# Kernel optimization log

Hardware: AMD Instinct MI355X
Metric: run time of the kernel (lower is better)

Reference implementation:

```python
import jax, jax.numpy as jnp
import numpy as np
import math

D_MODEL = 512
NHEAD = 8
HEAD_DIM = D_MODEL // NHEAD
MAX_REL = 128
B, T, S = 4, 2048, 2048


def setup_inputs() -> dict:
    key = jax.random.key(0)
    ks = jax.random.split(key, 16)
    sc = 1.0 / math.sqrt(D_MODEL)
    inp = {
        "query": jax.random.normal(ks[0], (B, T, D_MODEL), jnp.float32),
        "key": jax.random.normal(ks[1], (B, S, D_MODEL), jnp.float32),
        "value": jax.random.normal(ks[2], (B, S, D_MODEL), jnp.float32),
        "Wq": jax.random.normal(ks[3], (D_MODEL, D_MODEL), jnp.float32) * sc,
        "bq": jnp.zeros((D_MODEL,), jnp.float32),
        "Wk": jax.random.normal(ks[4], (D_MODEL, D_MODEL), jnp.float32) * sc,
        "bk": jnp.zeros((D_MODEL,), jnp.float32),
        "Wv": jax.random.normal(ks[5], (D_MODEL, D_MODEL), jnp.float32) * sc,
        "bv": jnp.zeros((D_MODEL,), jnp.float32),
        "Wo": jax.random.normal(ks[6], (D_MODEL, D_MODEL), jnp.float32) * sc,
        "bo": jnp.zeros((D_MODEL,), jnp.float32),
        "rel_emb": jax.random.normal(ks[7], (2 * MAX_REL + 1, NHEAD), jnp.float32) * 0.02,
    }
    return inp


def reference(query, key, value, Wq, bq, Wk, bk, Wv, bv, Wo, bo, rel_emb):
    # linear projections (torch Linear: x @ W.T + b), split heads -> [B,H,T,Dh]
    def proj(x, W, b, L):
        return (x @ W.T + b).reshape(B, L, NHEAD, HEAD_DIM).transpose(0, 2, 1, 3)

    q = proj(query, Wq, bq, T)
    k = proj(key, Wk, bk, S)
    v = proj(value, Wv, bv, S)

    scores = jnp.einsum("bhtd,bhsd->bhts", q, k) / math.sqrt(HEAD_DIM)

    # relative position bias lookup: rel[t,s] = clamp(t-s) + max_rel -> [H,T,S]
    rel = jnp.arange(T)[:, None] - jnp.arange(S)[None, :]
    rel = jnp.clip(rel, -MAX_REL, MAX_REL) + MAX_REL
    bias = rel_emb[rel].transpose(2, 0, 1)  # [H,T,S]
    scores = scores + bias[None]

    w = jax.nn.softmax(scores, axis=-1)  # dropout p used in eval mode -> identity
    out = jnp.einsum("bhts,bhsd->bhtd", w, v)
    out = out.transpose(0, 2, 1, 3).reshape(B, T, D_MODEL)
    return out @ Wo.T + bo
```

## Files before the change

kernel.cpp:

```cpp
#include <hip/hip_runtime.h>

typedef __attribute__((ext_vector_type(4))) float f32x4;
typedef __attribute__((ext_vector_type(16))) float f32x16;
typedef __attribute__((ext_vector_type(4))) unsigned short u16x4;
typedef __attribute__((ext_vector_type(8))) unsigned short u16x8;
typedef __attribute__((ext_vector_type(4))) unsigned int u32x4;
typedef __attribute__((ext_vector_type(8))) __bf16 bf16x8;

#define SZX_E ((size_t)4 * 2048 * 512)
#define SZW_E ((size_t)512 * 512)

__device__ __forceinline__ unsigned short f2bf(float f) {
  unsigned int u = __builtin_bit_cast(unsigned int, f);
  u += 0x7fffu + ((u >> 16) & 1u);
  return (unsigned short)(u >> 16);
}

__device__ __forceinline__ bf16x8 ld_bf8(const unsigned short* p) {
  return __builtin_bit_cast(bf16x8, *(const u16x8*)p);
}

__device__ __forceinline__ f32x4 mfma16(bf16x8 a, bf16x8 b, f32x4 c) {
  return __builtin_amdgcn_mfma_f32_16x16x32_bf16(a, b, c, 0, 0, 0);
}

__device__ __forceinline__ f32x16 mfma32(bf16x8 a, bf16x8 b, f32x16 c) {
  return __builtin_amdgcn_mfma_f32_32x32x16_bf16(a, b, c, 0, 0, 0);
}

__device__ __forceinline__ unsigned int cvt_pk_bf16(float lo, float hi) {
  unsigned int r;
  asm("v_cvt_pk_bf16_f32 %0, %1, %2" : "=v"(r) : "v"(lo), "v"(hi));
  return r;
}

__device__ __forceinline__ void plane32_swap(unsigned int& a, unsigned int& b) {
  asm("v_permlane32_swap_b32 %0, %1" : "+v"(a), "+v"(b));
}

__device__ __forceinline__ float exp2_fast(float x) {
  float r;
  asm("v_exp_f32 %0, %1" : "=v"(r) : "v"(x));
  return r;
}

__device__ __forceinline__ void gload16(const void* g, void* l) {
  __builtin_amdgcn_global_load_lds(
      (const __attribute__((address_space(1))) unsigned int*)g,
      (__attribute__((address_space(3))) unsigned int*)l, 16, 0, 0);
}

#define VBAR4 do { \
    asm volatile("s_waitcnt vmcnt(4)" ::: "memory"); \
    __builtin_amdgcn_sched_barrier(0); \
    __builtin_amdgcn_s_barrier(); \
    __builtin_amdgcn_sched_barrier(0); \
  } while (0)
#define VBAR0 do { \
    asm volatile("s_waitcnt vmcnt(0)" ::: "memory"); \
    __builtin_amdgcn_sched_barrier(0); \
    __builtin_amdgcn_s_barrier(); \
    __builtin_amdgcn_sched_barrier(0); \
  } while (0)

__global__ __launch_bounds__(256) void cvt_all(const float* __restrict__ q_,
                                               const float* __restrict__ k_,
                                               const float* __restrict__ v_,
                                               const float* __restrict__ wq_,
                                               const float* __restrict__ wk_,
                                               const float* __restrict__ wv_,
                                               const float* __restrict__ wo_,
                                               unsigned short* __restrict__ out) {
  const int bq = blockIdx.x;
  const float* src;
  size_t segbase, li;
  if (bq < 12288) {
    const int s = bq >> 12;
    src = (s == 0) ? q_ : (s == 1) ? k_ : v_;
    li = (size_t)(bq & 4095) * 256 + threadIdx.x;
    segbase = (size_t)s * 4194304;
  } else {
    const int s = (bq - 12288) >> 8;
    src = (s == 0) ? wq_ : (s == 1) ? wk_ : (s == 2) ? wv_ : wo_;
    li = (size_t)((bq - 12288) & 255) * 256 + threadIdx.x;
    segbase = 12582912 + (size_t)s * 262144;
  }
  const f32x4 v = *(const f32x4*)(src + li * 4);
  u16x4 r;
  r[0] = f2bf(v[0]); r[1] = f2bf(v[1]); r[2] = f2bf(v[2]); r[3] = f2bf(v[3]);
  *(u16x4*)(out + segbase + li * 4) = r;
}

__global__ __launch_bounds__(256) void gemm_qkv(const unsigned short* __restrict__ base,
                                                const float* __restrict__ bq,
                                                const float* __restrict__ bk,
                                                const float* __restrict__ bv,
                                                unsigned short* __restrict__ outb) {
  __shared__ unsigned short Asb[2][4096];
  __shared__ unsigned short Bsb[2][4096];
  const int z = blockIdx.z;
  const unsigned short* A = base + (size_t)z * SZX_E;
  const unsigned short* Bw = base + 3 * SZX_E + (size_t)z * SZW_E;
  const float* bias = (z == 0) ? bq : (z == 1) ? bk : bv;

  const int tid = threadIdx.x;
  const int l = tid & 63;
  const int w = tid >> 6;
  const int g = l >> 4;
  const int lr = l & 15;
  const int bid = blockIdx.x + (blockIdx.y << 2);
  const int lgg = (bid & 7) * 32 + (bid >> 3);
  const int nB = (lgg & 3) * 128;
  const int mB = (lgg >> 2) * 128;
  const int m0 = (w >> 1) * 64;
  const int n0 = (w & 1) * 64;
  const int ubase = tid & ~63;

  auto stage = [&](int bufi, int kk) {
#pragma unroll
    for (int i = 0; i < 2; i++) {
      const int idx = i * 256 + tid;
      const int ub = i * 256 + ubase;
      const int r = idx >> 2, c = idx & 3;
      gload16((const char*)A + ((size_t)(mB + r) * 512 + kk + c * 8) * 2,
              (char*)&Asb[bufi][0] + ub * 16);
      gload16((const char*)Bw + ((size_t)(nB + r) * 512 + kk + c * 8) * 2,
              (char*)&Bsb[bufi][0] + ub * 16);
    }
  };

  f32x4 acc[4][4];
#pragma unroll
  for (int i = 0; i < 4; i++)
#pragma unroll
    for (int j = 0; j < 4; j++) acc[i][j] = f32x4{0.f, 0.f, 0.f, 0.f};

  stage(0, 0);
  __syncthreads();
  int buf = 0;

  for (int ks = 0; ks < 16; ++ks) {
    if (ks < 15) stage(buf ^ 1, (ks + 1) * 32);
    bf16x8 af[4], bfr[4];
#pragma unroll
    for (int t = 0; t < 4; t++) {
      af[t] = ld_bf8(&Asb[buf][(m0 + t * 16 + lr) * 32 + g * 8]);
      bfr[t] = ld_bf8(&Bsb[buf][(n0 + t * 16 + lr) * 32 + g * 8]);
    }
#pragma unroll
    for (int i = 0; i < 4; i++)
#pragma unroll
      for (int j = 0; j < 4; j++)
        acc[i][j] = mfma16(af[i], bfr[j], acc[i][j]);
    __syncthreads();
    buf ^= 1;
  }

  unsigned short* outz = outb + (size_t)z * SZX_E;
#pragma unroll
  for (int j = 0; j < 4; j++) {
    const int n = nB + n0 + j * 16 + lr;
    const float bn = bias[n];
#pragma unroll
    for (int i = 0; i < 4; i++) {
#pragma unroll
      for (int r = 0; r < 4; r++) {
        const int m = mB + m0 + i * 16 + g * 4 + r;
        const float v = acc[i][j][r] + bn;
        if (z < 2) {
          outz[(size_t)m * 512 + n] = f2bf(v);
        } else {
          const int bb = m >> 11, s = m & 2047;
          const int hh = n >> 6, d = n & 63;
          outz[((size_t)((bb * 8 + hh) * 64 + d) << 11) + s] = f2bf(v);
        }
      }
    }
  }
}

__global__ __launch_bounds__(256) void gemm_o(const unsigned short* __restrict__ A,
                                              const unsigned short* __restrict__ Bw,
                                              const float* __restrict__ bias,
                                              float* __restrict__ Cout) {
  __shared__ unsigned short Asb[2][4096];
  __shared__ unsigned short Bsb[2][4096];
  const int tid = threadIdx.x;
  const int l = tid & 63;
  const int w = tid >> 6;
  const int g = l >> 4;
  const int lr = l & 15;
  const int bid = blockIdx.x + (blockIdx.y << 2);
  const int lgg = (bid & 7) * 32 + (bid >> 3);
  const int nB = (lgg & 3) * 128;
  const int mB = (lgg >> 2) * 128;
  const int m0 = (w >> 1) * 64;
  const int n0 = (w & 1) * 64;
  const int ubase = tid & ~63;

  auto stage = [&](int bufi, int kk) {
#pragma unroll
    for (int i = 0; i < 2; i++) {
      const int idx = i * 256 + tid;
      const int ub = i * 256 + ubase;
      const int r = idx >> 2, c = idx & 3;
      gload16((const char*)A + ((size_t)(mB + r) * 512 + kk + c * 8) * 2,
              (char*)&Asb[bufi][0] + ub * 16);
      gload16((const char*)Bw + ((size_t)(nB + r) * 512 + kk + c * 8) * 2,
              (char*)&Bsb[bufi][0] + ub * 16);
    }
  };

  f32x4 acc[4][4];
#pragma unroll
  for (int i = 0; i < 4; i++)
#pragma unroll
    for (int j = 0; j < 4; j++) acc[i][j] = f32x4{0.f, 0.f, 0.f, 0.f};

  stage(0, 0);
  __syncthreads();
  int buf = 0;

  for (int ks = 0; ks < 16; ++ks) {
    if (ks < 15) stage(buf ^ 1, (ks + 1) * 32);
    bf16x8 af[4], bfr[4];
#pragma unroll
    for (int t = 0; t < 4; t++) {
      af[t] = ld_bf8(&Asb[buf][(m0 + t * 16 + lr) * 32 + g * 8]);
      bfr[t] = ld_bf8(&Bsb[buf][(n0 + t * 16 + lr) * 32 + g * 8]);
    }
#pragma unroll
    for (int i = 0; i < 4; i++)
#pragma unroll
      for (int j = 0; j < 4; j++)
        acc[i][j] = mfma16(af[i], bfr[j], acc[i][j]);
    __syncthreads();
    buf ^= 1;
  }

#pragma unroll
  for (int j = 0; j < 4; j++) {
    const int n = nB + n0 + j * 16 + lr;
    const float bn = bias[n];
#pragma unroll
    for (int i = 0; i < 4; i++) {
#pragma unroll
      for (int r = 0; r < 4; r++) {
        const int m = mB + m0 + i * 16 + g * 4 + r;
        Cout[(size_t)m * 512 + n] = acc[i][j][r] + bn;
      }
    }
  }
}

__global__ __launch_bounds__(256, 2) void attn_kernel(const unsigned short* __restrict__ Qp,
                                                      const unsigned short* __restrict__ Kp,
                                                      const unsigned short* __restrict__ Vt,
                                                      const float* __restrict__ rel_emb,
                                                      unsigned short* __restrict__ At) {
  __shared__ float bias_s[257];
  __shared__ unsigned short K_lds[3][4096];
  __shared__ unsigned short V_lds[3][4096];
  const int bid0 = blockIdx.x;
  const int lg = (bid0 & 7) * 64 + (bid0 >> 3);
  const int qb = lg & 15;
  const int h = (lg >> 4) & 7;
  const int b = lg >> 7;
  const int tid = threadIdx.x;
  const int lane = tid & 63, w = tid >> 6;
  const int hi = lane >> 5, q31 = lane & 31;
  const int q0w = qb * 128 + w * 32;
  const int tq = q0w + q31;
  const float SCL = 0.125f * 1.44269504f;

  const bool isK = (w < 2);
  const char* sbase = isK ? (const char*)Kp + ((size_t)b * 2048 * 512 + h * 64) * 2
                          : (const char*)Vt + ((size_t)(b * 8 + h) * 64 * 2048) * 2;
  const size_t step = isK ? (size_t)64 * 1024 : 128;
  const int i0 = (w & 1) * 4;
  const int rr0 = (i0 + 0) * 8 + (lane >> 3), ch0 = (lane & 7) ^ (rr0 & 7);
  const int rr1 = (i0 + 1) * 8 + (lane >> 3), ch1 = (lane & 7) ^ (rr1 & 7);
  const int rr2 = (i0 + 2) * 8 + (lane >> 3), ch2 = (lane & 7) ^ (rr2 & 7);
  const int rr3 = (i0 + 3) * 8 + (lane >> 3), ch3 = (lane & 7) ^ (rr3 & 7);
  const size_t rstr = isK ? 1024 : 4096;
  const char* gp0 = sbase + (size_t)rr0 * rstr + ch0 * 16;
  const char* gp1 = sbase + (size_t)rr1 * rstr + ch1 * 16;
  const char* gp2 = sbase + (size_t)rr2 * rstr + ch2 * 16;
  const char* gp3 = sbase + (size_t)rr3 * rstr + ch3 * 16;
  char* dbA = (isK ? (char*)&K_lds[0][0] : (char*)&V_lds[0][0]) + i0 * 1024;
  char* dbB = (isK ? (char*)&K_lds[1][0] : (char*)&V_lds[1][0]) + i0 * 1024;
  char* dbC = (isK ? (char*)&K_lds[2][0] : (char*)&V_lds[2][0]) + i0 * 1024;

  auto STAGE = [&](char* dbase) {
    gload16(gp0, dbase);
    gload16(gp1, dbase + 1024);
    gload16(gp2, dbase + 2048);
    gload16(gp3, dbase + 3072);
    gp0 += step; gp1 += step; gp2 += step; gp3 += step;
  };

  const unsigned short* qptr = Qp + (size_t)(b * 2048 + tq) * 512 + h * 64 + hi * 8;
  const bf16x8 qf0 = ld_bf8(qptr);
  const bf16x8 qf1 = ld_bf8(qptr + 16);
  const bf16x8 qf2 = ld_bf8(qptr + 32);
  const bf16x8 qf3 = ld_bf8(qptr + 48);

  STAGE(dbA);
  STAGE(dbB);
  for (int i = tid; i < 257; i += 256) bias_s[i] = rel_emb[i * 8 + h] * 1.44269504f;
  __syncthreads();
  const float bias_lo = bias_s[0], bias_hi = bias_s[256];

  const int rswz = q31 & 7;
  int koff[4], voff[4];
#pragma unroll
  for (int c = 0; c < 4; c++) koff[c] = q31 * 64 + (((2 * c + hi) ^ rswz) << 3);
#pragma unroll
  for (int ks = 0; ks < 4; ks++) voff[ks] = q31 * 64 + (((ks * 2 + hi) ^ rswz) << 3);

  const f32x16 z16 = {0.f, 0.f, 0.f, 0.f, 0.f, 0.f, 0.f, 0.f,
                      0.f, 0.f, 0.f, 0.f, 0.f, 0.f, 0.f, 0.f};
  f32x16 o_lo = z16, o_hi = z16;
  float l_run = 0.f;

  auto TILE = [&](const unsigned short* kb, const unsigned short* vb, int s0) {
    bf16x8 kfl0 = ld_bf8(kb + koff[0]);
    bf16x8 kfh0 = ld_bf8(kb + 2048 + koff[0]);
    bf16x8 kfl1 = ld_bf8(kb + koff[1]);
    bf16x8 kfh1 = ld_bf8(kb + 2048 + koff[1]);
    bf16x8 kfl2 = ld_bf8(kb + koff[2]);
    bf16x8 kfh2 = ld_bf8(kb + 2048 + koff[2]);
    bf16x8 kfl3 = ld_bf8(kb + koff[3]);
    bf16x8 kfh3 = ld_bf8(kb + 2048 + koff[3]);
    bf16x8 vl[4], vh[4];
#pragma unroll
    for (int ks = 0; ks < 4; ks++) {
      vl[ks] = ld_bf8(vb + voff[ks]);
      vh[ks] = ld_bf8(vb + 2048 + voff[ks]);
    }

    f32x16 sa, sb;
    sa = mfma32(kfl0, qf0, z16);
    sb = mfma32(kfh0, qf0, z16);
    sa = mfma32(kfl1, qf1, sa);
    sb = mfma32(kfh1, qf1, sb);
    sa = mfma32(kfl2, qf2, sa);
    sb = mfma32(kfh2, qf2, sb);
    sa = mfma32(kfl3, qf3, sa);
    sb = mfma32(kfh3, qf3, sb);

    const int relmin = q0w - s0 - 63;
    const int relmax = q0w + 31 - s0;
    float SCL2, off0;
    if (relmin >= 128 || relmax <= -128) {
      SCL2 = SCL;
      off0 = (relmin >= 128) ? bias_hi : bias_lo;
    } else {
#pragma unroll
      for (int r = 0; r < 16; r++) {
        const int rowA = (r & 3) + 8 * (r >> 2) + 4 * hi;
        const int rA = tq - s0 - rowA;
        const int rB = rA - 32;
        const int iA = (rA < -128 ? -128 : (rA > 128 ? 128 : rA)) + 128;
        const int iB = (rB < -128 ? -128 : (rB > 128 ? 128 : rB)) + 128;
        sa[r] = fmaf(sa[r], SCL, bias_s[iA]);
        sb[r] = fmaf(sb[r], SCL, bias_s[iB]);
      }
      SCL2 = 1.f;
      off0 = 0.f;
    }

#pragma unroll
    for (int r = 0; r < 16; r++) {
      sa[r] = exp2_fast(fmaf(sa[r], SCL2, off0));
      sb[r] = exp2_fast(fmaf(sb[r], SCL2, off0));
    }
    float s8[8];
#pragma unroll
    for (int i = 0; i < 8; i++)
      s8[i] = (sa[i] + sa[i + 8]) + (sb[i] + sb[i + 8]);
    float ps = ((s8[0] + s8[1]) + (s8[2] + s8[3])) + ((s8[4] + s8[5]) + (s8[6] + s8[7]));
    ps += __shfl_xor(ps, 32, 64);
    l_run += ps;

    bf16x8 pa[4];
#pragma unroll
    for (int ks = 0; ks < 4; ks++) {
      const int c8 = (ks & 1) * 8;
      const f32x16& src = (ks < 2) ? sa : sb;
      unsigned int a0 = cvt_pk_bf16(src[c8 + 0], src[c8 + 1]);
      unsigned int b0 = cvt_pk_bf16(src[c8 + 4], src[c8 + 5]);
      unsigned int a1 = cvt_pk_bf16(src[c8 + 2], src[c8 + 3]);
      unsigned int b1 = cvt_pk_bf16(src[c8 + 6], src[c8 + 7]);
      plane32_swap(a0, b0);
      plane32_swap(a1, b1);
      pa[ks] = __builtin_bit_cast(bf16x8, u32x4{a0, a1, b0, b1});
    }

#pragma unroll
    for (int ks = 0; ks < 4; ks++) {
      o_lo = mfma32(pa[ks], vl[ks], o_lo);
      o_hi = mfma32(pa[ks], vh[ks], o_hi);
    }
  };

  const unsigned short* K0 = &K_lds[0][0];
  const unsigned short* K1 = &K_lds[1][0];
  const unsigned short* K2 = &K_lds[2][0];
  const unsigned short* V0 = &V_lds[0][0];
  const unsigned short* V1 = &V_lds[1][0];
  const unsigned short* V2 = &V_lds[2][0];

  for (int it = 0; it < 10; ++it) {
    const int u = it * 3;
    VBAR4; STAGE(dbC); TILE(K0, V0, u * 64);
    VBAR4; STAGE(dbA); TILE(K1, V1, (u + 1) * 64);
    VBAR4; STAGE(dbB); TILE(K2, V2, (u + 2) * 64);
  }
  VBAR4; TILE(K0, V0, 30 * 64);
  VBAR0; TILE(K1, V1, 31 * 64);

  const float inv = 1.f / l_run;
#pragma unroll
  for (int r2 = 0; r2 < 16; r2++) {
    const int ro = (r2 & 3) + 8 * (r2 >> 2) + 4 * hi;
    const float rr = __shfl(inv, ro, 64);
    unsigned short* op = At + (size_t)(b * 2048 + q0w + ro) * 512 + h * 64;
    op[q31] = f2bf(o_lo[r2] * rr);
    op[32 + q31] = f2bf(o_hi[r2] * rr);
  }
}

extern "C" void kernel_launch(void* const* d_in, const int* in_sizes, int n_in,
                              void* d_out, int out_size, void* d_ws, size_t ws_size,
                              hipStream_t stream) {
  const float* query = (const float*)d_in[0];
  const float* key   = (const float*)d_in[1];
  const float* value = (const float*)d_in[2];
  const float* Wq = (const float*)d_in[3];
  const float* bq = (const float*)d_in[4];
  const float* Wk = (const float*)d_in[5];
  const float* bk = (const float*)d_in[6];
  const float* Wv = (const float*)d_in[7];
  const float* bv = (const float*)d_in[8];
  const float* Wo = (const float*)d_in[9];
  const float* bo = (const float*)d_in[10];
  const float* rel = (const float*)d_in[11];

  char* ws = (char*)d_ws;
  unsigned short* base = (unsigned short*)ws;
  unsigned short* wo = base + 3 * SZX_E + 3 * SZW_E;
  unsigned short* Qp = base + 3 * SZX_E + 4 * SZW_E;
  unsigned short* Kp = Qp + SZX_E;
  unsigned short* Vt = Kp + SZX_E;
  unsigned short* At = Vt + SZX_E;

  cvt_all<<<dim3(13312), dim3(256), 0, stream>>>(query, key, value, Wq, Wk, Wv, Wo, base);

  dim3 blk(256);
  gemm_qkv<<<dim3(4, 64, 3), blk, 0, stream>>>(base, bq, bk, bv, Qp);

  attn_kernel<<<dim3(512), blk, 0, stream>>>(Qp, Kp, Vt, rel, At);

  gemm_o<<<dim3(4, 64), blk, 0, stream>>>(At, wo, bo, (float*)d_out);
}
```

Measured before the change: 102.0 us.

## Double attention block size to 8 waves sharing each K/V LDS tile

The attention kernel now launches 256 blocks of 512 threads, each covering 256 query rows instead of 128, so every K/V tile staged into LDS is reused by twice as many waves. Each wave now issues one K and one V load per stage, and the wait threshold drops from vmcnt(4) to vmcnt(2) to match. This halves global K/V traffic per query but gives only 256 blocks, which may not fill all CUs, and larger barriers may add sync cost. The bias init loop is adjusted to 512 threads with a redundant extra write of the last entry.

```diff
diff --git a/kernel.cpp b/kernel.cpp
--- a/kernel.cpp
+++ b/kernel.cpp
@@ -50,8 +50,8 @@
       (__attribute__((address_space(3))) unsigned int*)l, 16, 0, 0);
 }
 
-#define VBAR4 do { \
-    asm volatile("s_waitcnt vmcnt(4)" ::: "memory"); \
+#define VBAR2 do { \
+    asm volatile("s_waitcnt vmcnt(2)" ::: "memory"); \
     __builtin_amdgcn_sched_barrier(0); \
     __builtin_amdgcn_s_barrier(); \
     __builtin_amdgcn_sched_barrier(0); \
@@ -253,7 +253,7 @@
   }
 }
 
-__global__ __launch_bounds__(256, 2) void attn_kernel(const unsigned short* __restrict__ Qp,
+__global__ __launch_bounds__(512, 2) void attn_kernel(const unsigned short* __restrict__ Qp,
                                                       const unsigned short* __restrict__ Kp,
                                                       const unsigned short* __restrict__ Vt,
                                                       const float* __restrict__ rel_emb,
@@ -262,41 +262,31 @@
   __shared__ unsigned short K_lds[3][4096];
   __shared__ unsigned short V_lds[3][4096];
   const int bid0 = blockIdx.x;
-  const int lg = (bid0 & 7) * 64 + (bid0 >> 3);
-  const int qb = lg & 15;
-  const int h = (lg >> 4) & 7;
-  const int b = lg >> 7;
+  const int lg = (bid0 & 7) * 32 + (bid0 >> 3);
+  const int qb = lg & 7;
+  const int h = (lg >> 3) & 7;
+  const int b = lg >> 6;
   const int tid = threadIdx.x;
   const int lane = tid & 63, w = tid >> 6;
   const int hi = lane >> 5, q31 = lane & 31;
-  const int q0w = qb * 128 + w * 32;
+  const int q0w = qb * 256 + w * 32;
   const int tq = q0w + q31;
   const float SCL = 0.125f * 1.44269504f;
 
-  const bool isK = (w < 2);
-  const char* sbase = isK ? (const char*)Kp + ((size_t)b * 2048 * 512 + h * 64) * 2
-                          : (const char*)Vt + ((size_t)(b * 8 + h) * 64 * 2048) * 2;
-  const size_t step = isK ? (size_t)64 * 1024 : 128;
-  const int i0 = (w & 1) * 4;
-  const int rr0 = (i0 + 0) * 8 + (lane >> 3), ch0 = (lane & 7) ^ (rr0 & 7);
-  const int rr1 = (i0 + 1) * 8 + (lane >> 3), ch1 = (lane & 7) ^ (rr1 & 7);
-  const int rr2 = (i0 + 2) * 8 + (lane >> 3), ch2 = (lane & 7) ^ (rr2 & 7);
-  const int rr3 = (i0 + 3) * 8 + (lane >> 3), ch3 = (lane & 7) ^ (rr3 & 7);
-  const size_t rstr = isK ? 1024 : 4096;
-  const char* gp0 = sbase + (size_t)rr0 * rstr + ch0 * 16;
-  const char* gp1 = sbase + (size_t)rr1 * rstr + ch1 * 16;
-  const char* gp2 = sbase + (size_t)rr2 * rstr + ch2 * 16;
-  const char* gp3 = sbase + (size_t)rr3 * rstr + ch3 * 16;
-  char* dbA = (isK ? (char*)&K_lds[0][0] : (char*)&V_lds[0][0]) + i0 * 1024;
-  char* dbB = (isK ? (char*)&K_lds[1][0] : (char*)&V_lds[1][0]) + i0 * 1024;
-  char* dbC = (isK ? (char*)&K_lds[2][0] : (char*)&V_lds[2][0]) + i0 * 1024;
-
-  auto STAGE = [&](char* dbase) {
-    gload16(gp0, dbase);
-    gload16(gp1, dbase + 1024);
-    gload16(gp2, dbase + 2048);
-    gload16(gp3, dbase + 3072);
-    gp0 += step; gp1 += step; gp2 += step; gp3 += step;
+  const char* kstage = (const char*)Kp + ((size_t)b * 2048 * 512 + h * 64) * 2;
+  const char* vstage = (const char*)Vt + ((size_t)(b * 8 + h) * 64 * 2048) * 2;
+
+  const int rr = w * 8 + (lane >> 3);
+  const int ch = (lane & 7) ^ (rr & 7);
+  const char* gpK = kstage + (size_t)rr * 1024 + ch * 16;
+  const char* gpV = vstage + (size_t)rr * 4096 + ch * 16;
+  const int dslot = w * 1024;
+
+  auto STAGE = [&](int bufi) {
+    gload16(gpK, (char*)&K_lds[bufi][0] + dslot);
+    gload16(gpV, (char*)&V_lds[bufi][0] + dslot);
+    gpK += (size_t)64 * 1024;
+    gpV += 128;
   };
 
   const unsigned short* qptr = Qp + (size_t)(b * 2048 + tq) * 512 + h * 64 + hi * 8;
@@ -305,9 +295,10 @@
   const bf16x8 qf2 = ld_bf8(qptr + 32);
   const bf16x8 qf3 = ld_bf8(qptr + 48);
 
-  STAGE(dbA);
-  STAGE(dbB);
-  for (int i = tid; i < 257; i += 256) bias_s[i] = rel_emb[i * 8 + h] * 1.44269504f;
+  STAGE(0);
+  STAGE(1);
+  for (int i = tid; i < 257; i += 512) bias_s[i] = rel_emb[i * 8 + h] * 1.44269504f;
+  if (tid == 511) bias_s[256] = rel_emb[256 * 8 + h] * 1.44269504f;
   __syncthreads();
   const float bias_lo = bias_s[0], bias_hi = bias_s[256];
 
@@ -413,21 +404,21 @@
 
   for (int it = 0; it < 10; ++it) {
     const int u = it * 3;
-    VBAR4; STAGE(dbC); TILE(K0, V0, u * 64);
-    VBAR4; STAGE(dbA); TILE(K1, V1, (u + 1) * 64);
-    VBAR4; STAGE(dbB); TILE(K2, V2, (u + 2) * 64);
-  }
-  VBAR4; TILE(K0, V0, 30 * 64);
+    VBAR2; STAGE(2); TILE(K0, V0, u * 64);
+    VBAR2; STAGE(0); TILE(K1, V1, (u + 1) * 64);
+    VBAR2; STAGE(1); TILE(K2, V2, (u + 2) * 64);
+  }
+  VBAR2; TILE(K0, V0, 30 * 64);
   VBAR0; TILE(K1, V1, 31 * 64);
 
   const float inv = 1.f / l_run;
 #pragma unroll
   for (int r2 = 0; r2 < 16; r2++) {
     const int ro = (r2 & 3) + 8 * (r2 >> 2) + 4 * hi;
-    const float rr = __shfl(inv, ro, 64);
+    const float rr2 = __shfl(inv, ro, 64);
     unsigned short* op = At + (size_t)(b * 2048 + q0w + ro) * 512 + h * 64;
-    op[q31] = f2bf(o_lo[r2] * rr);
-    op[32 + q31] = f2bf(o_hi[r2] * rr);
+    op[q31] = f2bf(o_lo[r2] * rr2);
+    op[32 + q31] = f2bf(o_hi[r2] * rr2);
   }
 }
 
@@ -460,7 +451,7 @@
   dim3 blk(256);
   gemm_qkv<<<dim3(4, 64, 3), blk, 0, stream>>>(base, bq, bk, bv, Qp);
 
-  attn_kernel<<<dim3(512), blk, 0, stream>>>(Qp, Kp, Vt, rel, At);
+  attn_kernel<<<dim3(256), dim3(512), 0, stream>>>(Qp, Kp, Vt, rel, At);
 
   gemm_o<<<dim3(4, 64), blk, 0, stream>>>(At, wo, bo, (float*)d_out);
 }
```

Measured after the change: 104.0 us. About the same (+2.0%).
